# Kernel tuning notes

Measured on AMD Instinct MI355X. Metric: run time of the kernel, lower is better.

## Reference

```python
import jax, jax.numpy as jnp
import numpy as np

B, T, V, D, U, NT = 32, 512, 32000, 300, 300, 3


def setup_inputs() -> dict:
    key = jax.random.key(0)
    ks = jax.random.split(key, 10)
    s = 0.05
    return {
        "inputs": jax.random.randint(ks[0], (B, T), 0, V),
        "sequence_length": jax.random.randint(ks[1], (B,), 0, T),
        "emb": jax.random.normal(ks[2], (V, D), jnp.float32) * s,
        "Wk_f": jax.random.normal(ks[3], (D, 4 * U), jnp.float32) * s,
        "Wr_f": jax.random.normal(ks[4], (U, 4 * U), jnp.float32) * s,
        "b_f": jnp.zeros((4 * U,), jnp.float32),
        "Wk_b": jax.random.normal(ks[5], (D, 4 * U), jnp.float32) * s,
        "Wr_b": jax.random.normal(ks[6], (U, 4 * U), jnp.float32) * s,
        "b_b": jnp.zeros((4 * U,), jnp.float32),
        "fc_W": jax.random.normal(ks[7], (2 * U, NT), jnp.float32) * s,
        "fc_b": jnp.zeros((NT,), jnp.float32),
    }


def _lstm_scan(x, mask, Wk, Wr, b):
    # x: [B,T,D], mask: [B,T] bool. Keras semantics: masked steps carry h,c through.
    units = Wr.shape[0]
    zx = jnp.einsum('btd,dz->btz', x, Wk) + b        # precompute input projection
    zx_t = jnp.swapaxes(zx, 0, 1)                    # [T,B,4U]
    m_t = jnp.swapaxes(mask, 0, 1)                   # [T,B]

    def step(carry, inp):
        h, c = carry
        zxt, mt = inp
        z = zxt + h @ Wr                             # [B,4U]
        i, f, g, o = jnp.split(z, 4, axis=-1)
        c_new = jax.nn.sigmoid(f) * c + jax.nn.sigmoid(i) * jnp.tanh(g)
        h_new = jax.nn.sigmoid(o) * jnp.tanh(c_new)
        m = mt[:, None]
        h = jnp.where(m, h_new, h)
        c = jnp.where(m, c_new, c)
        return (h, c), h

    h0 = jnp.zeros((x.shape[0], units), x.dtype)
    _, hs = jax.lax.scan(step, (h0, h0), (zx_t, m_t))
    return jnp.swapaxes(hs, 0, 1)                    # [B,T,U]


def reference(inputs, sequence_length, emb, Wk_f, Wr_f, b_f, Wk_b, Wr_b, b_b, fc_W, fc_b):
    x = emb[inputs]                                   # [B,T,D]
    mask = jnp.arange(T)[None, :] < sequence_length[:, None]  # [B,T]
    h_fwd = _lstm_scan(x, mask, Wk_f, Wr_f, b_f)
    # backward direction: reverse time (input + mask), scan, reverse output back
    h_bwd = jnp.flip(_lstm_scan(jnp.flip(x, 1), jnp.flip(mask, 1), Wk_b, Wr_b, b_b), 1)
    h = jnp.concatenate([h_fwd, h_bwd], axis=-1)      # [B,T,2U]
    return h @ fc_W + fc_b                            # [B,T,NT]
```

## Files before the change

### kernel.cpp

```cpp
#include <hip/hip_runtime.h>
#include <stdint.h>


#define BB 32
#define TT 512
#define DD 300
#define UU 300
#define G4 1200
#define NTOK 3

#define KB   10
#define UPB  30
#define NCOL 120
#define KTILES 10
#define HSTR 320
#define HROW 304

#define WKROWS 1280
#define WKSTR  320

typedef uint16_t bf16_t;
typedef short  s16x8 __attribute__((ext_vector_type(8)));
typedef float  f32x4 __attribute__((ext_vector_type(4)));

union U8 { unsigned long long q[2]; s16x8 v; };

__device__ __forceinline__ float bf2f(uint16_t u) {
    union { uint32_t i; float f; } v; v.i = ((uint32_t)u) << 16; return v.f;
}
__device__ __forceinline__ uint16_t f2bf(float f) {
    union { uint32_t i; float f; } v; v.f = f;
    uint32_t r = v.i + 0x7fffu + ((v.i >> 16) & 1u);
    return (uint16_t)(r >> 16);
}
__device__ __forceinline__ float ldf(const void* base, size_t idx, int f32m) {
    return f32m ? ((const float*)base)[idx]
                : bf2f(((const uint16_t*)base)[idx]);
}

__device__ __forceinline__ f32x4 xpose4(f32x4 v, int lane) {
    f32x4 t, w, s, r;
    t[0] = __shfl_xor(v[0], 1); t[1] = __shfl_xor(v[1], 1);
    t[2] = __shfl_xor(v[2], 1); t[3] = __shfl_xor(v[3], 1);
    if ((lane & 1) == 0) { w[0]=v[0]; w[1]=t[0]; w[2]=v[2]; w[3]=t[2]; }
    else                 { w[0]=t[1]; w[1]=v[1]; w[2]=t[3]; w[3]=v[3]; }
    s[0] = __shfl_xor(w[0], 2); s[1] = __shfl_xor(w[1], 2);
    s[2] = __shfl_xor(w[2], 2); s[3] = __shfl_xor(w[3], 2);
    if ((lane & 2) == 0) { r[0]=w[0]; r[1]=w[1]; r[2]=s[0]; r[3]=s[1]; }
    else                 { r[0]=s[2]; r[1]=s[3]; r[2]=w[2]; r[3]=w[3]; }
    return r;
}

__device__ __forceinline__ void gatefn(f32x4 zv, uint2 zp, bool m,
                                       float& c, float& h) {
    float zi = zv[0] + bf2f((uint16_t)(zp.x & 0xffff));
    float zf = zv[1] + bf2f((uint16_t)(zp.x >> 16));
    float zg = zv[2] + bf2f((uint16_t)(zp.y & 0xffff));
    float zo = zv[3] + bf2f((uint16_t)(zp.y >> 16));
    float si = 1.f / (1.f + __expf(-zi));
    float sf = 1.f / (1.f + __expf(-zf));
    float so = 1.f / (1.f + __expf(-zo));
    float tg = tanhf(zg);
    float cn = sf * c + si * tg;
    float hn = so * tanhf(cn);
    if (m) { c = cn; h = hn; }
}

__global__ void detect_dtype(const uint16_t* __restrict__ emb_u16,
                             int* __restrict__ flag) {
    __shared__ float red[256];
    const int tid = threadIdx.x;
    float m = 0.f;
    for (int k = tid; k < 4096; k += 256)
        m = fmaxf(m, fabsf(bf2f(emb_u16[2 * k])));
    red[tid] = m;
    __syncthreads();
    for (int s = 128; s > 0; s >>= 1) {
        if (tid < s) red[tid] = fmaxf(red[tid], red[tid + s]);
        __syncthreads();
    }
    if (tid == 0) flag[0] = (red[0] > 1.0e3f) ? 1 : 0;
}

__global__ void prep_wrp(const void* __restrict__ Wr_f,
                         const void* __restrict__ Wr_b,
                         bf16_t* __restrict__ WrPT_f,
                         bf16_t* __restrict__ WrPT_b,
                         const int* __restrict__ flagp) {
    const int f32m = *flagp;
    int idx = blockIdx.x * 256 + threadIdx.x;
    const void* src = blockIdx.y ? Wr_b : Wr_f;
    bf16_t*     dst = blockIdx.y ? WrPT_b : WrPT_f;
    if (idx < G4 * HROW) {
        int p = idx / HROW;
        int k = idx - p * HROW;
        int u = p >> 2, g = p & 3;
        float v = (k < DD) ? ldf(src, (size_t)k * G4 + g * UU + u, f32m) : 0.f;
        dst[idx] = f2bf(v);
    }
}

__global__ void prep_wkt(const void* __restrict__ Wk_f, const void* __restrict__ b_f,
                         const void* __restrict__ Wk_b, const void* __restrict__ b_b,
                         bf16_t* __restrict__ WkT, bf16_t* __restrict__ biasP,
                         const int* __restrict__ flagp) {
    const int f32m = *flagp;
    const int dir = blockIdx.y;
    const void* Wk = dir ? Wk_b : Wk_f;
    const void* bs = dir ? b_b  : b_f;
    bf16_t* dst = WkT + (size_t)dir * (WKROWS * WKSTR);
    int idx = blockIdx.x * 256 + threadIdx.x;
    if (idx < WKROWS * WKSTR) {
        int p = idx / WKSTR;
        int k = idx - p * WKSTR;
        int u = p >> 2, g = p & 3;
        float v = (p < G4 && k < DD) ? ldf(Wk, (size_t)k * G4 + g * UU + u, f32m)
                                     : 0.f;
        dst[idx] = f2bf(v);
        if (idx < WKROWS) {
            int pp = idx, uu = pp >> 2, gg = pp & 3;
            biasP[dir * WKROWS + idx] =
                (pp < G4) ? f2bf(ldf(bs, gg * UU + uu, f32m)) : (bf16_t)0;
        }
    }
}

__global__ void init_state(bf16_t* __restrict__ Hglob, int* __restrict__ flags) {
    int i = blockIdx.x * 256 + threadIdx.x;
    if (i < 2 * 2 * BB * HROW) Hglob[i] = 0;
    if (i < 2 * TT * 16) flags[i] = 0;
}

#define ZM 64
#define ZN 128
__global__ __launch_bounds__(256, 2) void zx_gemm2(
    const int* __restrict__ inputs, const void* __restrict__ emb,
    const bf16_t* __restrict__ WkTall, const bf16_t* __restrict__ biasP,
    bf16_t* __restrict__ zxf, bf16_t* __restrict__ zxb,
    const int* __restrict__ flagp) {

    const int f32m = *flagp;
    const int dir = blockIdx.z;
    const bf16_t* WkT = WkTall + (size_t)dir * (WKROWS * WKSTR);
    const bf16_t* bp  = biasP + dir * WKROWS;
    bf16_t* out = dir ? zxb : zxf;

    const int tid = threadIdx.x;
    const int pb = blockIdx.x * ZN;
    const int rowBase = blockIdx.y * ZM;

    __shared__ __align__(16) uint16_t Alds[ZM * HSTR];
    __shared__ int rowids[ZM];

    if (tid < ZM) rowids[tid] = inputs[rowBase + tid];
    for (int i = tid; i < ZM * HSTR; i += 256) Alds[i] = 0;
    __syncthreads();

    for (int i = tid; i < ZM * 38; i += 256) {
        int r = i / 38, g = i - 38 * r;
        int k0 = g * 8;
        const size_t eb = (size_t)rowids[r] * DD + k0;
        uint16_t tmp[8];
        if (g < 37) {
            if (f32m) {
                const float* ef = (const float*)emb + eb;
#pragma unroll
                for (int e = 0; e < 8; e++) tmp[e] = f2bf(ef[e]);
            } else {
                *(uint4*)tmp = *(const uint4*)((const uint16_t*)emb + eb);
            }
        } else {
#pragma unroll
            for (int e = 0; e < 8; e++) {
                int k = k0 + e;
                tmp[e] = (k < DD)
                    ? (f32m ? f2bf(((const float*)emb)[(size_t)rowids[r] * DD + k])
                            : ((const uint16_t*)emb)[(size_t)rowids[r] * DD + k])
                    : (uint16_t)0;
            }
        }
        *(uint4*)&Alds[r * HSTR + ((g ^ (r & 7)) << 3)] = *(uint4*)tmp;
    }
    __syncthreads();

    const int lane = tid & 63;
    const int wv   = tid >> 6;
    const int q    = lane >> 4;
    const int c16  = lane & 15;
    const int n0   = 32 * wv;
    const int sw7  = c16 & 7;

    f32x4 acc[4][2];
#pragma unroll
    for (int mt = 0; mt < 4; mt++)
        for (int nh = 0; nh < 2; nh++) acc[mt][nh] = (f32x4){0.f,0.f,0.f,0.f};

    const int p0 = pb + n0 + c16;
    const int p1 = p0 + 16;
#pragma unroll
    for (int kt = 0; kt < KTILES; kt++) {
        int k0 = 32 * kt + 8 * q;
        int sw = (((kt * 4 + q) ^ sw7) << 3);
        s16x8 b0 = *(const s16x8*)&WkT[(size_t)p0 * WKSTR + k0];
        s16x8 b1 = *(const s16x8*)&WkT[(size_t)p1 * WKSTR + k0];
#pragma unroll
        for (int mt = 0; mt < 4; mt++) {
            s16x8 af = *(const s16x8*)&Alds[(16 * mt + c16) * HSTR + sw];
            acc[mt][0] = __builtin_amdgcn_mfma_f32_16x16x32_bf16(af, b0, acc[mt][0], 0, 0, 0);
            acc[mt][1] = __builtin_amdgcn_mfma_f32_16x16x32_bf16(af, b1, acc[mt][1], 0, 0, 0);
        }
    }

    __syncthreads();
    float* Cs = (float*)Alds;
#pragma unroll
    for (int mt = 0; mt < 4; mt++)
#pragma unroll
        for (int nh = 0; nh < 2; nh++)
#pragma unroll
            for (int r = 0; r < 4; r++)
                Cs[(16 * mt + 4 * q + r) * 132 + n0 + 16 * nh + c16] = acc[mt][nh][r];
    __syncthreads();

    for (int i = tid; i < ZM * (ZN / 2); i += 256) {
        int r = i >> 6, cc = (i & 63) * 2;
        int p = pb + cc;
        if (p < G4) {
            float v0 = Cs[r * 132 + cc]     + bf2f(bp[p]);
            float v1 = Cs[r * 132 + cc + 1] + bf2f(bp[p + 1]);
            uint32_t pk = (uint32_t)f2bf(v0) | ((uint32_t)f2bf(v1) << 16);
            *(uint32_t*)&out[(size_t)(rowBase + r) * G4 + p] = pk;
        }
    }
}

__global__ __launch_bounds__(256, 1) void lstm_rec4(
    const bf16_t* __restrict__ zxf, const bf16_t* __restrict__ zxb,
    const bf16_t* __restrict__ WrPT_f, const bf16_t* __restrict__ WrPT_b,
    const int* __restrict__ seqlen,
    bf16_t* __restrict__ Hglob, int* __restrict__ flags,
    bf16_t* __restrict__ hf, bf16_t* __restrict__ hb) {

    const int blk = blockIdx.x % KB;
    const int dir = blockIdx.x / KB;
    const bf16_t* zx   = dir ? zxb    : zxf;
    const bf16_t* WrPT = dir ? WrPT_b : WrPT_f;
    bf16_t*       hout = dir ? hb : hf;
    bf16_t*       Hg   = Hglob + (size_t)dir * (2 * BB * HROW);
    int*          fbase = flags + dir * (TT * 16);

    __shared__ __align__(16) uint16_t Hlds[BB * HSTR];
    __shared__ uint16_t hstage[BB * UPB];

    const int tid  = threadIdx.x;
    const int lane = tid & 63;
    const int wv   = tid >> 6;
    const int q    = lane >> 4;
    const int c16  = lane & 15;
    const int n0   = 32 * wv;
    const int sw7  = c16 & 7;
    const int k4   = c16 >> 2;
    const int j4   = c16 & 3;
    const int u0   = 8 * wv + k4;
    const int b0   = 4 * q + j4;
    const bool v1  = (u0 + 4 < UPB);
    const bool pollme = (lane < KB) && (lane != blk);

    for (int i = tid; i < BB * HSTR; i += 256) Hlds[i] = 0;
    U8 Bf0[KTILES], Bf1[KTILES];
#pragma unroll
    for (int kt = 0; kt < KTILES; kt++) {
        int k0 = 32 * kt + 8 * q;
        int col0 = n0 + c16, col1 = n0 + 16 + c16;
        U8 z; z.q[0] = 0; z.q[1] = 0;
        Bf0[kt] = z; Bf1[kt] = z;
        if (k0 < 304) {
            if (col0 < NCOL)
                Bf0[kt].v = *(const s16x8*)&WrPT[(size_t)(NCOL * blk + col0) * HROW + k0];
            if (col1 < NCOL)
                Bf1[kt].v = *(const s16x8*)&WrPT[(size_t)(NCOL * blk + col1) * HROW + k0];
        }
    }
    float c00 = 0.f, c01 = 0.f, c10 = 0.f, c11 = 0.f;
    float h00 = 0.f, h01 = 0.f, h10 = 0.f, h11 = 0.f;
    const int L0 = seqlen[b0];
    const int L1 = seqlen[b0 + 16];
    __syncthreads();

    for (int ts = 0; ts < TT; ts++) {
        const int t = dir ? (TT - 1 - ts) : ts;

        const size_t zr0 = ((size_t)(b0 * TT + t)) * G4 + NCOL * blk;
        const size_t zr1 = ((size_t)((b0 + 16) * TT + t)) * G4 + NCOL * blk;
        uint2 z00 = *(const uint2*)&zx[zr0 + 4 * u0];
        uint2 z10 = *(const uint2*)&zx[zr1 + 4 * u0];
        uint2 z01 = {0, 0}, z11 = {0, 0};
        if (v1) {
            z01 = *(const uint2*)&zx[zr0 + 4 * (u0 + 4)];
            z11 = *(const uint2*)&zx[zr1 + 4 * (u0 + 4)];
        }

        if (ts > 0) {
            int* fl = fbase + (ts - 1) * 16;
            for (;;) {
                int v = pollme ? __hip_atomic_load(&fl[lane], __ATOMIC_RELAXED,
                                                   __HIP_MEMORY_SCOPE_AGENT)
                               : 1;
                if (__all(v != 0)) break;
                __builtin_amdgcn_s_sleep(1);
            }
        }

        const unsigned long long* Hsrc64 =
            (const unsigned long long*)(Hg + (size_t)(ts & 1) * (BB * HROW));
        unsigned long long hv[10];
#pragma unroll
        for (int k = 0; k < 9; k++)
            hv[k] = __hip_atomic_load(&Hsrc64[tid + 256 * k], __ATOMIC_RELAXED,
                                      __HIP_MEMORY_SCOPE_AGENT);
        if (tid < 128)
            hv[9] = __hip_atomic_load(&Hsrc64[2304 + tid], __ATOMIC_RELAXED,
                                      __HIP_MEMORY_SCOPE_AGENT);
#pragma unroll
        for (int k = 0; k < 9; k++) {
            int i = tid + 256 * k;
            int b = i / 76, x = i - 76 * b;
            *(unsigned long long*)
                &Hlds[b * HSTR + ((((x >> 1) ^ (b & 7)) << 3) | ((x & 1) << 2))]
                = hv[k];
        }
        if (tid < 128) {
            int i = 2304 + tid;
            int b = i / 76, x = i - 76 * b;
            *(unsigned long long*)
                &Hlds[b * HSTR + ((((x >> 1) ^ (b & 7)) << 3) | ((x & 1) << 2))]
                = hv[9];
        }
        __syncthreads();

        f32x4 acc00 = {0.f,0.f,0.f,0.f}, acc01 = {0.f,0.f,0.f,0.f};
        f32x4 acc10 = {0.f,0.f,0.f,0.f}, acc11 = {0.f,0.f,0.f,0.f};
#pragma unroll
        for (int kt = 0; kt < KTILES; kt++) {
            int sw = (((kt * 4 + q) ^ sw7) << 3);
            s16x8 a0 = *(const s16x8*)&Hlds[c16 * HSTR + sw];
            s16x8 a1 = *(const s16x8*)&Hlds[(c16 + 16) * HSTR + sw];
            acc00 = __builtin_amdgcn_mfma_f32_16x16x32_bf16(a0, Bf0[kt].v, acc00, 0, 0, 0);
            acc01 = __builtin_amdgcn_mfma_f32_16x16x32_bf16(a0, Bf1[kt].v, acc01, 0, 0, 0);
            acc10 = __builtin_amdgcn_mfma_f32_16x16x32_bf16(a1, Bf0[kt].v, acc10, 0, 0, 0);
            acc11 = __builtin_amdgcn_mfma_f32_16x16x32_bf16(a1, Bf1[kt].v, acc11, 0, 0, 0);
        }

        f32x4 t00 = xpose4(acc00, lane);
        f32x4 t01 = xpose4(acc01, lane);
        f32x4 t10 = xpose4(acc10, lane);
        f32x4 t11 = xpose4(acc11, lane);
        const bool m0 = (t < L0);
        const bool m1 = (t < L1);
        gatefn(t00, z00, m0, c00, h00);
        gatefn(t01, z01, m0, c01, h01);
        gatefn(t10, z10, m1, c10, h10);
        gatefn(t11, z11, m1, c11, h11);

        hstage[b0 * UPB + u0]        = f2bf(h00);
        hstage[(b0 + 16) * UPB + u0] = f2bf(h10);
        if (v1) {
            hstage[b0 * UPB + u0 + 4]        = f2bf(h01);
            hstage[(b0 + 16) * UPB + u0 + 4] = f2bf(h11);
        }
        __syncthreads();

        if (ts < TT - 1) {
            bf16_t* Hdst = Hg + (size_t)((ts + 1) & 1) * (BB * HROW);
            for (int i = tid; i < BB * (UPB / 2); i += 256) {
                int b = i / (UPB / 2), k = i - b * (UPB / 2);
                uint32_t val = (uint32_t)hstage[b * UPB + 2 * k] |
                               ((uint32_t)hstage[b * UPB + 2 * k + 1] << 16);
                __hip_atomic_store(
                    (uint32_t*)&Hdst[b * HROW + UPB * blk + 2 * k], val,
                    __ATOMIC_RELAXED, __HIP_MEMORY_SCOPE_AGENT);
            }
            __syncthreads();
            if (tid == 0)
                __hip_atomic_store(&fbase[ts * 16 + blk], 1, __ATOMIC_RELAXED,
                                   __HIP_MEMORY_SCOPE_AGENT);
        }

        for (int i = tid; i < BB * (UPB / 2); i += 256) {
            int b = i / (UPB / 2), k = i - b * (UPB / 2);
            uint32_t val = (uint32_t)hstage[b * UPB + 2 * k] |
                           ((uint32_t)hstage[b * UPB + 2 * k + 1] << 16);
            *(uint32_t*)&hout[((size_t)(b * TT + t)) * UU + UPB * blk + 2 * k] = val;
        }
    }
}

__global__ __launch_bounds__(256) void fc_out(
    const bf16_t* __restrict__ hf, const bf16_t* __restrict__ hb,
    const void* __restrict__ fcW, const void* __restrict__ fcb,
    void* __restrict__ out, const int* __restrict__ flagp) {

    const int f32m = *flagp;
    __shared__ float W[2 * UU * NTOK];
    __shared__ float bias[NTOK];
    const int tid = threadIdx.x;
    for (int i = tid; i < 2 * UU * NTOK; i += 256) W[i] = ldf(fcW, i, f32m);
    if (tid < NTOK) bias[tid] = ldf(fcb, tid, f32m);
    __syncthreads();

    const int r = blockIdx.x * 256 + tid;
    const bf16_t* hfr = hf + (size_t)r * UU;
    const bf16_t* hbr = hb + (size_t)r * UU;
    float s0 = bias[0], s1 = bias[1], s2 = bias[2];
    for (int u = 0; u < UU; u++) {
        float f = bf2f(hfr[u]);
        s0 += f * W[u * 3 + 0];
        s1 += f * W[u * 3 + 1];
        s2 += f * W[u * 3 + 2];
    }
    for (int u = 0; u < UU; u++) {
        float f = bf2f(hbr[u]);
        s0 += f * W[(UU + u) * 3 + 0];
        s1 += f * W[(UU + u) * 3 + 1];
        s2 += f * W[(UU + u) * 3 + 2];
    }
    if (f32m) {
        float* o = (float*)out;
        o[(size_t)r * 3 + 0] = s0;
        o[(size_t)r * 3 + 1] = s1;
        o[(size_t)r * 3 + 2] = s2;
    } else {
        bf16_t* o = (bf16_t*)out;
        o[(size_t)r * 3 + 0] = f2bf(s0);
        o[(size_t)r * 3 + 1] = f2bf(s1);
        o[(size_t)r * 3 + 2] = f2bf(s2);
    }
}

extern "C" void kernel_launch(void* const* d_in, const int* in_sizes, int n_in,
                              void* d_out, int out_size, void* d_ws, size_t ws_size,
                              hipStream_t stream) {
    const int* inputs = (const int*)d_in[0];
    const int* seqlen = (const int*)d_in[1];
    const void* emb  = d_in[2];
    const void* Wk_f = d_in[3];
    const void* Wr_f = d_in[4];
    const void* b_f  = d_in[5];
    const void* Wk_b = d_in[6];
    const void* Wr_b = d_in[7];
    const void* b_b  = d_in[8];
    const void* fcW  = d_in[9];
    const void* fcb  = d_in[10];

    char* ws = (char*)d_ws;
    int*    flag   = (int*)(ws + 0);
    int*    flags  = (int*)(ws + 64);
    bf16_t* Hglob  = (bf16_t*)(ws + 65664);
    bf16_t* WrPT_f = (bf16_t*)(ws + 143488);
    bf16_t* WrPT_b = (bf16_t*)(ws + 873088);
    bf16_t* zxPf   = (bf16_t*)(ws + 1602688);
    bf16_t* zxPb   = (bf16_t*)(ws + 40924288);
    bf16_t* hfbuf  = (bf16_t*)(ws + 80245888);
    bf16_t* hbbuf  = (bf16_t*)(ws + 90076288);
    bf16_t* WkT    = hfbuf;
    bf16_t* biasP  = hfbuf + 2 * WKROWS * WKSTR;

    detect_dtype<<<1, 256, 0, stream>>>((const uint16_t*)emb, flag);
    {
        dim3 grid((G4 * HROW + 255) / 256, 2);
        prep_wrp<<<grid, 256, 0, stream>>>(Wr_f, Wr_b, WrPT_f, WrPT_b, flag);
    }
    {
        dim3 grid((WKROWS * WKSTR + 255) / 256, 2);
        prep_wkt<<<grid, 256, 0, stream>>>(Wk_f, b_f, Wk_b, b_b, WkT, biasP, flag);
    }
    init_state<<<64, 256, 0, stream>>>(Hglob, flags);
    {
        dim3 grid(10, 256, 2);
        zx_gemm2<<<grid, 256, 0, stream>>>(inputs, emb, WkT, biasP,
                                           zxPf, zxPb, flag);
    }
    lstm_rec4<<<2 * KB, 256, 0, stream>>>(zxPf, zxPb, WrPT_f, WrPT_b, seqlen,
                                          Hglob, flags, hfbuf, hbbuf);
    fc_out<<<(BB * TT) / 256, 256, 0, stream>>>(hfbuf, hbbuf, fcW, fcb,
                                                d_out, flag);
}
```

Measured before the change: 2.068 ms.

## Replace flag-based inter-block sync with tagged hidden-state words in LSTM recurrence

The recurrent kernel no longer uses a separate per-step flag array and barrier-then-flag publish. Each block now writes its h slice as 64-bit words carrying a step tag in the upper half. Consumers poll the data words directly until every tag matches, which removes a global round trip and a __syncthreads per step. The unit partition is also changed to 32 units per block, so the last block does padded work, and the hout store is merged into the same pass as the publish. The cost is doubled traffic for the exchanged state and repeated reloads of all words while polling.

```diff
diff --git a/kernel.cpp b/kernel.cpp
--- a/kernel.cpp
+++ b/kernel.cpp
@@ -10,14 +10,18 @@
 #define NTOK 3
 
 #define KB   10
-#define UPB  30
-#define NCOL 120
+#define UPB  32
+#define NCOL 128
 #define KTILES 10
 #define HSTR 320
 #define HROW 304
 
 #define WKROWS 1280
 #define WKSTR  320
+
+#define WPR  150
+#define WBUF (BB * WPR)
+#define PW   19
 
 typedef uint16_t bf16_t;
 typedef short  s16x8 __attribute__((ext_vector_type(8)));
@@ -125,10 +129,9 @@
     }
 }
 
-__global__ void init_state(bf16_t* __restrict__ Hglob, int* __restrict__ flags) {
+__global__ void init_state(unsigned long long* __restrict__ Hw) {
     int i = blockIdx.x * 256 + threadIdx.x;
-    if (i < 2 * 2 * BB * HROW) Hglob[i] = 0;
-    if (i < 2 * TT * 16) flags[i] = 0;
+    if (i < 2 * 2 * WBUF) Hw[i] = 0ull;
 }
 
 #define ZM 64
@@ -234,11 +237,11 @@
     }
 }
 
-__global__ __launch_bounds__(256, 1) void lstm_rec4(
+__global__ __launch_bounds__(256, 1) void lstm_rec5(
     const bf16_t* __restrict__ zxf, const bf16_t* __restrict__ zxb,
     const bf16_t* __restrict__ WrPT_f, const bf16_t* __restrict__ WrPT_b,
     const int* __restrict__ seqlen,
-    bf16_t* __restrict__ Hglob, int* __restrict__ flags,
+    unsigned long long* __restrict__ Hw,
     bf16_t* __restrict__ hf, bf16_t* __restrict__ hb) {
 
     const int blk = blockIdx.x % KB;
@@ -246,11 +249,10 @@
     const bf16_t* zx   = dir ? zxb    : zxf;
     const bf16_t* WrPT = dir ? WrPT_b : WrPT_f;
     bf16_t*       hout = dir ? hb : hf;
-    bf16_t*       Hg   = Hglob + (size_t)dir * (2 * BB * HROW);
-    int*          fbase = flags + dir * (TT * 16);
+    unsigned long long* const Hwd = Hw + (size_t)dir * (2 * WBUF);
 
     __shared__ __align__(16) uint16_t Hlds[BB * HSTR];
-    __shared__ uint16_t hstage[BB * UPB];
+    __shared__ __align__(8)  uint16_t hstage[BB * UPB];
 
     const int tid  = threadIdx.x;
     const int lane = tid & 63;
@@ -263,22 +265,40 @@
     const int j4   = c16 & 3;
     const int u0   = 8 * wv + k4;
     const int b0   = 4 * q + j4;
-    const bool v1  = (u0 + 4 < UPB);
-    const bool pollme = (lane < KB) && (lane != blk);
+    const int ug0  = UPB * blk + u0;
+    const bool real0 = (ug0     < DD);
+    const bool real1 = (ug0 + 4 < DD);
+    const size_t zco0 = 4 * (size_t)(real0 ? ug0 : 0);
+    const size_t zco1 = 4 * (size_t)(real1 ? (ug0 + 4) : 0);
+    const int jmax = (blk < KB - 1) ? 16 : 6;
+    const int jj   = tid & 15;
+    const int brow = tid >> 4;
+
+    int Wl[PW], El[PW];
+#pragma unroll
+    for (int m = 0; m < PW; ++m) {
+        int W = tid + 256 * m;
+        if (W >= WBUF) W = tid;
+        int b = W / WPR, j = W - WPR * b;
+        int u = 2 * j, g = u >> 3;
+        Wl[m] = W;
+        El[m] = b * HSTR + ((g ^ (b & 7)) << 3) + (u & 7);
+    }
 
     for (int i = tid; i < BB * HSTR; i += 256) Hlds[i] = 0;
     U8 Bf0[KTILES], Bf1[KTILES];
 #pragma unroll
     for (int kt = 0; kt < KTILES; kt++) {
         int k0 = 32 * kt + 8 * q;
-        int col0 = n0 + c16, col1 = n0 + 16 + c16;
+        int p0g = NCOL * blk + n0 + c16;
+        int p1g = p0g + 16;
         U8 z; z.q[0] = 0; z.q[1] = 0;
         Bf0[kt] = z; Bf1[kt] = z;
-        if (k0 < 304) {
-            if (col0 < NCOL)
-                Bf0[kt].v = *(const s16x8*)&WrPT[(size_t)(NCOL * blk + col0) * HROW + k0];
-            if (col1 < NCOL)
-                Bf1[kt].v = *(const s16x8*)&WrPT[(size_t)(NCOL * blk + col1) * HROW + k0];
+        if (k0 < HROW) {
+            if (p0g < G4)
+                Bf0[kt].v = *(const s16x8*)&WrPT[(size_t)p0g * HROW + k0];
+            if (p1g < G4)
+                Bf1[kt].v = *(const s16x8*)&WrPT[(size_t)p1g * HROW + k0];
         }
     }
     float c00 = 0.f, c01 = 0.f, c10 = 0.f, c11 = 0.f;
@@ -290,51 +310,30 @@
     for (int ts = 0; ts < TT; ts++) {
         const int t = dir ? (TT - 1 - ts) : ts;
 
-        const size_t zr0 = ((size_t)(b0 * TT + t)) * G4 + NCOL * blk;
-        const size_t zr1 = ((size_t)((b0 + 16) * TT + t)) * G4 + NCOL * blk;
-        uint2 z00 = *(const uint2*)&zx[zr0 + 4 * u0];
-        uint2 z10 = *(const uint2*)&zx[zr1 + 4 * u0];
-        uint2 z01 = {0, 0}, z11 = {0, 0};
-        if (v1) {
-            z01 = *(const uint2*)&zx[zr0 + 4 * (u0 + 4)];
-            z11 = *(const uint2*)&zx[zr1 + 4 * (u0 + 4)];
-        }
+        const size_t zr0 = ((size_t)(b0 * TT + t)) * G4;
+        const size_t zr1 = ((size_t)((b0 + 16) * TT + t)) * G4;
+        uint2 z00 = *(const uint2*)&zx[zr0 + zco0];
+        uint2 z10 = *(const uint2*)&zx[zr1 + zco0];
+        uint2 z01 = *(const uint2*)&zx[zr0 + zco1];
+        uint2 z11 = *(const uint2*)&zx[zr1 + zco1];
 
         if (ts > 0) {
-            int* fl = fbase + (ts - 1) * 16;
-            for (;;) {
-                int v = pollme ? __hip_atomic_load(&fl[lane], __ATOMIC_RELAXED,
-                                                   __HIP_MEMORY_SCOPE_AGENT)
-                               : 1;
-                if (__all(v != 0)) break;
-                __builtin_amdgcn_s_sleep(1);
-            }
-        }
-
-        const unsigned long long* Hsrc64 =
-            (const unsigned long long*)(Hg + (size_t)(ts & 1) * (BB * HROW));
-        unsigned long long hv[10];
-#pragma unroll
-        for (int k = 0; k < 9; k++)
-            hv[k] = __hip_atomic_load(&Hsrc64[tid + 256 * k], __ATOMIC_RELAXED,
-                                      __HIP_MEMORY_SCOPE_AGENT);
-        if (tid < 128)
-            hv[9] = __hip_atomic_load(&Hsrc64[2304 + tid], __ATOMIC_RELAXED,
-                                      __HIP_MEMORY_SCOPE_AGENT);
-#pragma unroll
-        for (int k = 0; k < 9; k++) {
-            int i = tid + 256 * k;
-            int b = i / 76, x = i - 76 * b;
-            *(unsigned long long*)
-                &Hlds[b * HSTR + ((((x >> 1) ^ (b & 7)) << 3) | ((x & 1) << 2))]
-                = hv[k];
-        }
-        if (tid < 128) {
-            int i = 2304 + tid;
-            int b = i / 76, x = i - 76 * b;
-            *(unsigned long long*)
-                &Hlds[b * HSTR + ((((x >> 1) ^ (b & 7)) << 3) | ((x & 1) << 2))]
-                = hv[9];
+            const unsigned long long* const src = Hwd + (size_t)(ts & 1) * WBUF;
+            const uint32_t tagv = (uint32_t)ts;
+            uint32_t mask = (1u << PW) - 1;
+            do {
+                unsigned long long v[PW];
+#pragma unroll
+                for (int m = 0; m < PW; ++m)
+                    v[m] = __hip_atomic_load(&src[Wl[m]], __ATOMIC_RELAXED,
+                                             __HIP_MEMORY_SCOPE_AGENT);
+#pragma unroll
+                for (int m = 0; m < PW; ++m)
+                    if ((mask & (1u << m)) && (uint32_t)(v[m] >> 32) == tagv) {
+                        *(uint32_t*)&Hlds[El[m]] = (uint32_t)v[m];
+                        mask &= ~(1u << m);
+                    }
+            } while (__any(mask != 0));
         }
         __syncthreads();
 
@@ -362,35 +361,29 @@
         gatefn(t10, z10, m1, c10, h10);
         gatefn(t11, z11, m1, c11, h11);
 
-        hstage[b0 * UPB + u0]        = f2bf(h00);
-        hstage[(b0 + 16) * UPB + u0] = f2bf(h10);
-        if (v1) {
-            hstage[b0 * UPB + u0 + 4]        = f2bf(h01);
-            hstage[(b0 + 16) * UPB + u0 + 4] = f2bf(h11);
-        }
+        hstage[b0 * UPB + u0]            = real0 ? f2bf(h00) : (uint16_t)0;
+        hstage[(b0 + 16) * UPB + u0]     = real0 ? f2bf(h10) : (uint16_t)0;
+        hstage[b0 * UPB + u0 + 4]        = real1 ? f2bf(h01) : (uint16_t)0;
+        hstage[(b0 + 16) * UPB + u0 + 4] = real1 ? f2bf(h11) : (uint16_t)0;
         __syncthreads();
 
-        if (ts < TT - 1) {
-            bf16_t* Hdst = Hg + (size_t)((ts + 1) & 1) * (BB * HROW);
-            for (int i = tid; i < BB * (UPB / 2); i += 256) {
-                int b = i / (UPB / 2), k = i - b * (UPB / 2);
-                uint32_t val = (uint32_t)hstage[b * UPB + 2 * k] |
-                               ((uint32_t)hstage[b * UPB + 2 * k + 1] << 16);
-                __hip_atomic_store(
-                    (uint32_t*)&Hdst[b * HROW + UPB * blk + 2 * k], val,
-                    __ATOMIC_RELAXED, __HIP_MEMORY_SCOPE_AGENT);
+        if (jj < jmax) {
+            uint32_t p0 = *(const uint32_t*)&hstage[brow * UPB + 2 * jj];
+            uint32_t p1 = *(const uint32_t*)&hstage[(brow + 16) * UPB + 2 * jj];
+            if (ts < TT - 1) {
+                unsigned long long* const dst =
+                    Hwd + (size_t)((ts + 1) & 1) * WBUF;
+                const unsigned long long tg =
+                    ((unsigned long long)(uint32_t)(ts + 1)) << 32;
+                __hip_atomic_store(&dst[brow * WPR + 16 * blk + jj], tg | p0,
+                                   __ATOMIC_RELAXED, __HIP_MEMORY_SCOPE_AGENT);
+                __hip_atomic_store(&dst[(brow + 16) * WPR + 16 * blk + jj], tg | p1,
+                                   __ATOMIC_RELAXED, __HIP_MEMORY_SCOPE_AGENT);
             }
-            __syncthreads();
-            if (tid == 0)
-                __hip_atomic_store(&fbase[ts * 16 + blk], 1, __ATOMIC_RELAXED,
-                                   __HIP_MEMORY_SCOPE_AGENT);
-        }
-
-        for (int i = tid; i < BB * (UPB / 2); i += 256) {
-            int b = i / (UPB / 2), k = i - b * (UPB / 2);
-            uint32_t val = (uint32_t)hstage[b * UPB + 2 * k] |
-                           ((uint32_t)hstage[b * UPB + 2 * k + 1] << 16);
-            *(uint32_t*)&hout[((size_t)(b * TT + t)) * UU + UPB * blk + 2 * k] = val;
+            *(uint32_t*)&hout[((size_t)(brow * TT + t)) * UU
+                              + UPB * blk + 2 * jj] = p0;
+            *(uint32_t*)&hout[((size_t)((brow + 16) * TT + t)) * UU
+                              + UPB * blk + 2 * jj] = p1;
         }
     }
 }
@@ -454,14 +447,13 @@
 
     char* ws = (char*)d_ws;
     int*    flag   = (int*)(ws + 0);
-    int*    flags  = (int*)(ws + 64);
-    bf16_t* Hglob  = (bf16_t*)(ws + 65664);
-    bf16_t* WrPT_f = (bf16_t*)(ws + 143488);
-    bf16_t* WrPT_b = (bf16_t*)(ws + 873088);
-    bf16_t* zxPf   = (bf16_t*)(ws + 1602688);
-    bf16_t* zxPb   = (bf16_t*)(ws + 40924288);
-    bf16_t* hfbuf  = (bf16_t*)(ws + 80245888);
-    bf16_t* hbbuf  = (bf16_t*)(ws + 90076288);
+    unsigned long long* Hw = (unsigned long long*)(ws + 64);
+    bf16_t* WrPT_f = (bf16_t*)(ws + 153664);
+    bf16_t* WrPT_b = (bf16_t*)(ws + 883264);
+    bf16_t* zxPf   = (bf16_t*)(ws + 1612864);
+    bf16_t* zxPb   = (bf16_t*)(ws + 40934464);
+    bf16_t* hfbuf  = (bf16_t*)(ws + 80256064);
+    bf16_t* hbbuf  = (bf16_t*)(ws + 90086464);
     bf16_t* WkT    = hfbuf;
     bf16_t* biasP  = hfbuf + 2 * WKROWS * WKSTR;
 
@@ -474,14 +466,14 @@
         dim3 grid((WKROWS * WKSTR + 255) / 256, 2);
         prep_wkt<<<grid, 256, 0, stream>>>(Wk_f, b_f, Wk_b, b_b, WkT, biasP, flag);
     }
-    init_state<<<64, 256, 0, stream>>>(Hglob, flags);
+    init_state<<<75, 256, 0, stream>>>(Hw);
     {
         dim3 grid(10, 256, 2);
         zx_gemm2<<<grid, 256, 0, stream>>>(inputs, emb, WkT, biasP,
                                            zxPf, zxPb, flag);
     }
-    lstm_rec4<<<2 * KB, 256, 0, stream>>>(zxPf, zxPb, WrPT_f, WrPT_b, seqlen,
-                                          Hglob, flags, hfbuf, hbbuf);
+    lstm_rec5<<<2 * KB, 256, 0, stream>>>(zxPf, zxPb, WrPT_f, WrPT_b, seqlen,
+                                          Hw, hfbuf, hbbuf);
     fc_out<<<(BB * TT) / 256, 256, 0, stream>>>(hfbuf, hbbuf, fcW, fcb,
                                                 d_out, flag);
 }
```

Measured after the change: 2.195 ms. 1.06x slower.
